# Performance work log

Hardware: AMD Instinct MI355X
Metric: run time of the kernel (lower is better)

## Reference

```python
import jax, jax.numpy as jnp
import numpy as np

H = 256
NUM_REL = 460
NUM_ENT = 20000
B = 4096
CUR_TS = 10
PATH_LEN = 8


def _gru_step(x, h, W_ih, W_hh, b_ih, b_hh):
    # PyTorch GRUCell math
    gi = x @ W_ih.T + b_ih          # [B, 3H]
    gh = h @ W_hh.T + b_hh          # [B, 3H]
    ir, iz, inn = jnp.split(gi, 3, axis=1)
    hr, hz, hn = jnp.split(gh, 3, axis=1)
    r = jax.nn.sigmoid(ir + hr)
    z = jax.nn.sigmoid(iz + hz)
    n = jnp.tanh(inn + r * hn)
    return (1.0 - z) * n + z * h


def setup_inputs() -> dict:
    key = jax.random.key(0)
    ks = jax.random.split(key, 24)
    s = 1.0 / np.sqrt(H)
    f32 = jnp.float32
    d = {
        "pre_emb": jax.random.normal(ks[0], (NUM_ENT, H), f32),
        "r_emb": jax.random.normal(ks[1], (NUM_REL, H), f32),
        "partial_embeding": jax.random.normal(ks[2], (B, CUR_TS * NUM_REL), f32),
        # params (uniform-ish linear init scaled by 1/sqrt(H))
        "W_map1": jax.random.normal(ks[3], (2 * H, H), f32) * s,
        "b_map1": jax.random.normal(ks[4], (2 * H,), f32) * s,
        "W_map2": jax.random.normal(ks[5], (H, 2 * H), f32) * s,
        "b_map2": jax.random.normal(ks[6], (H,), f32) * s,
        "W_h1": jax.random.normal(ks[7], (H, H), f32) * s,
        "b_h1": jax.random.normal(ks[8], (H,), f32) * s,
        "W_h2": jax.random.normal(ks[9], (H, H), f32) * s,
        "b_h2": jax.random.normal(ks[10], (H,), f32) * s,
        "W_attn": jax.random.normal(ks[11], (H, H), f32) * s,
        "b_attn": jax.random.normal(ks[12], (H,), f32) * s,
        "W_align": jax.random.normal(ks[13], (H, H), f32) * s,
        "b_align": jax.random.normal(ks[14], (H,), f32) * s,
        "W_ih": jax.random.normal(ks[15], (3 * H, H), f32) * s,
        "W_hh": jax.random.normal(ks[16], (3 * H, H), f32) * s,
        "b_ih": jax.random.normal(ks[17], (3 * H,), f32) * s,
        "b_hh": jax.random.normal(ks[18], (3 * H,), f32) * s,
        "all_triples": jax.random.randint(ks[19], (B, 3), 0, NUM_REL, dtype=jnp.int64)
        if jax.config.jax_enable_x64 else jax.random.randint(ks[19], (B, 3), 0, NUM_REL, dtype=jnp.int32),
        "cur_ts": CUR_TS,
        "num_rel": NUM_REL,
    }
    return d


def reference(pre_emb, r_emb, partial_embeding,
              W_map1, b_map1, W_map2, b_map2,
              W_h1, b_h1, W_h2, b_h2,
              W_attn, b_attn, W_align, b_align,
              W_ih, W_hh, b_ih, b_hh,
              all_triples, cur_ts, num_rel):
    # rel_mapping1 -> rel_mapping2
    mapped_rel = (r_emb @ W_map1.T + b_map1) @ W_map2.T + b_map2     # [R, H]
    q_rel = mapped_rel[all_triples[:, 1]]                            # [B, H]

    # attention logits base (constant over timesteps): linear_attn(q_rel) @ mapped_rel.T
    attn_base = (q_rel @ W_attn.T + b_attn) @ mapped_rel.T           # [B, R]

    start_ts = max(cur_ts - PATH_LEN, 0)
    nb = partial_embeding.shape[0]
    cur_seq = partial_embeding.reshape(nb, cur_ts, num_rel)[:, start_ts:cur_ts]  # [B, T, R]
    cur_seq = jnp.swapaxes(cur_seq, 0, 1)                            # [T, B, R]

    h0 = jnp.zeros((nb, H), dtype=pre_emb.dtype)

    def step(h, cur):
        attn = cur * attn_base
        attn = jnp.where(attn == 0, jnp.asarray(-1e9, attn.dtype), attn)
        attn = jax.nn.softmax(attn, axis=1)
        x = attn @ mapped_rel                                        # [B, H]
        return _gru_step(x, h, W_ih, W_hh, b_ih, b_hh), None

    gru_hidden, _ = jax.lax.scan(step, h0, cur_seq)

    # predicted history embedding + match loss (MSE)
    predicted_hist = 0.1 * ((q_rel @ W_h1.T + b_h1) @ W_h2.T + b_h2) + q_rel
    match_loss = jnp.mean((predicted_hist - gru_hidden) ** 2)

    # forward_forth, distmult scoring
    h2 = _gru_step(q_rel, predicted_hist, W_ih, W_hh, b_ih, b_hh)    # [B, H]
    aligned_all = pre_emb @ W_align.T + b_align                      # [E, H]
    sub = aligned_all[all_triples[:, 0]]                             # [B, H]
    score_logits = (sub * h2) @ aligned_all.T                        # [B, E]
    score = jax.nn.sigmoid(score_logits)

    # BCE(sigmoid(logits), one_hot(obj)) in stable logits form without
    # materializing the dense one-hot label matrix:
    # mean over B*E of [ softplus(x) - x * label ]
    obj = all_triples[:, 2]
    pos_logits = score_logits[jnp.arange(nb), obj]
    path_loss = (jnp.sum(jax.nn.softplus(score_logits)) - jnp.sum(pos_logits)) / (nb * score_logits.shape[1])

    return match_loss, path_loss, score
```

## Files before the change

### kernel.cpp

```cpp
#include <hip/hip_runtime.h>
#include <hip/hip_bf16.h>

typedef __hip_bfloat16 bf16;
typedef __attribute__((ext_vector_type(8))) short short8;
typedef __attribute__((ext_vector_type(4))) float f32x4;
typedef __attribute__((ext_vector_type(4))) short short4v;

#define NREL 460
#define KP   480
#define NENT 20000
#define NENT_PAD 20096
#define NB   4096

__device__ inline float sigmoidf_(float x){ return 1.f/(1.f+__expf(-x)); }

__device__ inline void gload16(const bf16* g, bf16* l){
  __builtin_amdgcn_global_load_lds(
      (const __attribute__((address_space(1))) unsigned int*)g,
      (__attribute__((address_space(3))) unsigned int*)l, 16, 0, 0);
}

__device__ __forceinline__ void fgemm_body(
    const float* __restrict__ A, int lda, int arows,
    const float* __restrict__ B, int ldb,
    const float* __restrict__ bias,
    float* __restrict__ C, int ldc, int K, int mode,
    const float* __restrict__ add_src, bf16* __restrict__ ct_out,
    int bx, int by)
{
  __shared__ __align__(16) float As[32][68];
  __shared__ __align__(16) float Bs[32][68];
  const int tid = threadIdx.x;
  const int row0 = bx*64, col0 = by*64;
  const int tx = tid & 15, ty = tid >> 4;
  float acc[4][4] = {};
  for (int k0 = 0; k0 < K; k0 += 32){
    __syncthreads();
    #pragma unroll
    for (int s = 0; s < 2; ++s){
      int slot = tid + s*256;
      int r = slot >> 3, c4 = (slot & 7)*4;
      int ra = row0 + r; if (ra >= arows) ra = arows - 1;
      float4 v = *(const float4*)(A + (long)ra*lda + k0 + c4);
      As[c4+0][r] = v.x; As[c4+1][r] = v.y; As[c4+2][r] = v.z; As[c4+3][r] = v.w;
      float4 w = *(const float4*)(B + (long)(col0 + r)*ldb + k0 + c4);
      Bs[c4+0][r] = w.x; Bs[c4+1][r] = w.y; Bs[c4+2][r] = w.z; Bs[c4+3][r] = w.w;
    }
    __syncthreads();
    #pragma unroll
    for (int kk = 0; kk < 32; ++kk){
      float4 a4 = *(const float4*)(&As[kk][ty*4]);
      float4 b4 = *(const float4*)(&Bs[kk][tx*4]);
      float av[4] = {a4.x, a4.y, a4.z, a4.w};
      float bv[4] = {b4.x, b4.y, b4.z, b4.w};
      #pragma unroll
      for (int i = 0; i < 4; ++i)
        #pragma unroll
        for (int j = 0; j < 4; ++j) acc[i][j] += av[i]*bv[j];
    }
  }
  const int rb = row0 + ty*4, cb = col0 + tx*4;
  if (mode == 1){
    #pragma unroll
    for (int i = 0; i < 4; ++i){
      float4 v = {acc[i][0], acc[i][1], acc[i][2], acc[i][3]};
      *(float4*)(C + (long)(rb+i)*ldc + cb) = v;
      int rr = rb + i;
      if (rr < KP){
        #pragma unroll
        for (int j = 0; j < 4; ++j)
          ct_out[(cb+j)*KP + rr] = __float2bfloat16(rr < NREL ? acc[i][j] : 0.f);
      }
    }
  } else if (mode == 2){
    #pragma unroll
    for (int i = 0; i < 4; ++i){
      float4 v;
      #pragma unroll
      for (int j = 0; j < 4; ++j)
        ((float*)&v)[j] = 0.1f*(acc[i][j] + bias[cb+j]) + add_src[(long)(rb+i)*ldc + cb+j];
      *(float4*)(C + (long)(rb+i)*ldc + cb) = v;
    }
  } else {
    float bv[4] = {0,0,0,0};
    if (bias){ bv[0]=bias[cb]; bv[1]=bias[cb+1]; bv[2]=bias[cb+2]; bv[3]=bias[cb+3]; }
    #pragma unroll
    for (int i = 0; i < 4; ++i){
      float4 v = {acc[i][0]+bv[0], acc[i][1]+bv[1], acc[i][2]+bv[2], acc[i][3]+bv[3]};
      *(float4*)(C + (long)(rb+i)*ldc + cb) = v;
    }
  }
}

__global__ __launch_bounds__(256) void k_fgemm(
    const float* A, int lda, int arows, const float* B, int ldb,
    const float* bias, float* C, int ldc, int K, int mode,
    const float* add_src, bf16* ct_out){
  fgemm_body(A, lda, arows, B, ldb, bias, C, ldc, K, mode, add_src, ct_out,
             blockIdx.x, blockIdx.y);
}

struct FDesc {
  const float* A; const float* B; const float* bias; float* C;
  const float* add; bf16* ct;
  int lda, ldb, ldc, K, arows, mode;
};

__global__ __launch_bounds__(256) void k_fgemm_multi(FDesc d0, FDesc d1, FDesc d2,
                                                     int y1, int y2){
  int y = blockIdx.y;
  FDesc d; int by;
  if (y < y1){ d = d0; by = y; }
  else if (y < y2){ d = d1; by = y - y1; }
  else { d = d2; by = y - y2; }
  fgemm_body(d.A, d.lda, d.arows, d.B, d.ldb, d.bias, d.C, d.ldc, d.K, d.mode,
             d.add, d.ct, blockIdx.x, by);
}

__global__ __launch_bounds__(256) void k_h2(const float* __restrict__ M_ih,
    const float* __restrict__ b_ih, const float* __restrict__ ghp,
    const float* __restrict__ ph, float* __restrict__ h2_rel){
  int r = blockIdx.x, c = threadIdx.x;
  float rg = sigmoidf_(M_ih[r*768+c]       + b_ih[c]       + ghp[r*768+c]);
  float zg = sigmoidf_(M_ih[r*768+256+c]   + b_ih[256+c]   + ghp[r*768+256+c]);
  float ng = tanhf    (M_ih[r*768+512+c]   + b_ih[512+c]   + rg*ghp[r*768+512+c]);
  h2_rel[r*256+c] = (1.f - zg)*ng + zg*ph[r*256+c];
}

__global__ void k_f2bf3(const float4* __restrict__ s0, short4v* __restrict__ d0, int n0,
                        const float4* __restrict__ s1, short4v* __restrict__ d1, int n1,
                        const float4* __restrict__ s2, short4v* __restrict__ d2, int n2,
                        short4v* __restrict__ pad0, int n3, double* __restrict__ dz){
  int i = blockIdx.x*256 + threadIdx.x;
  if (i < n0+n1+n2){
    const float4* s; short4v* d; int j;
    if (i < n0){ s = s0; d = d0; j = i; }
    else if (i < n0+n1){ s = s1; d = d1; j = i-n0; }
    else { s = s2; d = d2; j = i-n0-n1; }
    float4 v = s[j];
    bf16 a = __float2bfloat16(v.x), b = __float2bfloat16(v.y);
    bf16 c = __float2bfloat16(v.z), e = __float2bfloat16(v.w);
    short4v o; o.x = *(short*)&a; o.y = *(short*)&b; o.z = *(short*)&c; o.w = *(short*)&e;
    d[j] = o;
  } else if (i < n0+n1+n2+n3){
    short4v z = {0,0,0,0};
    pad0[i - (n0+n1+n2)] = z;
  } else if (i < n0+n1+n2+n3+4){
    dz[i - (n0+n1+n2+n3)] = 0.0;
  }
}

__global__ __launch_bounds__(256) void k_soft_makep(const float* __restrict__ partial,
    const float* __restrict__ attn_base, const int* __restrict__ trips,
    bf16* __restrict__ attn_all,
    const bf16* __restrict__ Qbf, const float* __restrict__ h2_rel,
    bf16* __restrict__ P){
  int bid = blockIdx.x;
  if (bid >= NB/4){
    int i = (bid - NB/4)*256 + threadIdx.x;
    int b = i >> 8, k = i & 255;
    int s = trips[b*3+0], rel = trips[b*3+1];
    P[i] = __float2bfloat16(__bfloat162float(Qbf[s*256+k]) * h2_rel[rel*256+k]);
    return;
  }
  int wave = threadIdx.x >> 6, lane = threadIdx.x & 63;
  int b = bid*4 + wave;
  int rel = trips[b*3+1];
  const float* base = attn_base + (long)rel*512;
  float bs[8];
  #pragma unroll
  for (int s = 0; s < 8; ++s){
    int idx = s*64 + lane;
    bs[s] = (idx < NREL) ? base[idx] : 0.f;
  }
  const float* cur0 = partial + (long)b*4600 + 2*NREL;
  for (int t = 0; t < 8; ++t){
    const float* cur = cur0 + t*NREL;
    float v[8]; float mx = -1e30f;
    #pragma unroll
    for (int s = 0; s < 8; ++s){
      int idx = s*64 + lane;
      float val = -1e30f;
      if (idx < NREL){
        float pz = cur[idx]*bs[s];
        val = (pz == 0.f) ? -1e9f : pz;
      }
      v[s] = val; mx = fmaxf(mx, val);
    }
    #pragma unroll
    for (int off = 32; off >= 1; off >>= 1) mx = fmaxf(mx, __shfl_xor(mx, off));
    float sum = 0.f;
    #pragma unroll
    for (int s = 0; s < 8; ++s){
      int idx = s*64 + lane;
      if (idx < NREL){ v[s] = __expf(v[s]-mx); sum += v[s]; }
    }
    #pragma unroll
    for (int off = 32; off >= 1; off >>= 1) sum += __shfl_xor(sum, off);
    float inv = 1.f/sum;
    long obase = ((long)t*NB + b)*KP;
    #pragma unroll
    for (int s = 0; s < 8; ++s){
      int idx = s*64 + lane;
      if (idx < KP) attn_all[obase + idx] = __float2bfloat16(idx < NREL ? v[s]*inv : 0.f);
    }
  }
}

template<int MODE>
__global__ __launch_bounds__(256) void k_gemm128(
    const bf16* __restrict__ A, int lda,
    const bf16* __restrict__ B, int ldb,
    const float* __restrict__ bias,
    void* __restrict__ C, long ldc,
    int K, int n_valid, double* __restrict__ sp_sum,
    const int* __restrict__ trips)
{
  __shared__ __align__(16) bf16 sbuf[16384];
  __shared__ float wsum[8];
  const int tid = threadIdx.x;
  const int lane = tid & 63, wave = tid >> 6;
  const long row0 = (long)blockIdx.x * 128;
  const long col0 = (long)blockIdx.y * 128;
  const int sr = tid >> 2;
  const int sc = (tid & 3) * 8;
  const bf16* Ag0 = A + (row0 + sr)*lda + sc;
  const bf16* Ag1 = A + (row0 + 64 + sr)*lda + sc;
  const bf16* Bg0 = B + (col0 + sr)*ldb + sc;
  const bf16* Bg1 = B + (col0 + 64 + sr)*ldb + sc;
  const int wr = (wave >> 1)*64, wc = (wave & 1)*64;
  const int rA = lane & 15, kA = (lane >> 4)*8;
  f32x4 acc[4][4] = {};
  const int nt = K >> 5;
  bf16* As_ = sbuf;
  bf16* Bs_ = sbuf + 8192;
  gload16(Ag0, As_ + tid*8);
  gload16(Ag1, As_ + 2048 + tid*8);
  gload16(Bg0, Bs_ + tid*8);
  gload16(Bg1, Bs_ + 2048 + tid*8);
  int cur = 0;
  for (int t = 0; t < nt; ++t){
    if (t + 1 < nt){
      const int k0 = (t+1) << 5;
      const int nxt = cur ^ 1;
      gload16(Ag0 + k0, As_ + nxt*4096 + tid*8);
      gload16(Ag1 + k0, As_ + nxt*4096 + 2048 + tid*8);
      gload16(Bg0 + k0, Bs_ + nxt*4096 + tid*8);
      gload16(Bg1 + k0, Bs_ + nxt*4096 + 2048 + tid*8);
      asm volatile("s_waitcnt vmcnt(4)" ::: "memory");
    } else {
      asm volatile("s_waitcnt vmcnt(0)" ::: "memory");
    }
    __builtin_amdgcn_s_barrier();
    short8 a[4], b[4];
    #pragma unroll
    for (int m = 0; m < 4; ++m) a[m] = *(const short8*)(As_ + cur*4096 + (wr + m*16 + rA)*32 + kA);
    #pragma unroll
    for (int n = 0; n < 4; ++n) b[n] = *(const short8*)(Bs_ + cur*4096 + (wc + n*16 + rA)*32 + kA);
    asm volatile("s_waitcnt lgkmcnt(0)" ::: "memory");
    __builtin_amdgcn_s_barrier();
    #pragma unroll
    for (int m = 0; m < 4; ++m)
      #pragma unroll
      for (int n = 0; n < 4; ++n)
        acc[m][n] = __builtin_amdgcn_mfma_f32_16x16x32_bf16(a[m], b[n], acc[m][n], 0,0,0);
    cur ^= 1;
  }
  const int ri = (lane >> 4)*4, ci = lane & 15;
  __syncthreads();
  if constexpr (MODE == 1){
    bf16* epi = sbuf + wave*1152;
    const int rrow = lane >> 2, q = lane & 3;
    #pragma unroll
    for (int m = 0; m < 4; ++m){
      #pragma unroll
      for (int n = 0; n < 4; ++n){
        long c = col0 + wc + n*16 + ci;
        float bv = bias ? bias[c] : 0.f;
        #pragma unroll
        for (int i = 0; i < 4; ++i)
          epi[(ri+i)*72 + n*16 + ci] = __float2bfloat16(acc[m][n][i] + bv);
      }
      long gr = row0 + wr + m*16 + rrow;
      bf16* gp = (bf16*)C + gr*ldc + col0 + wc + q*16;
      const bf16* lp = epi + rrow*72 + q*16;
      *(short8*)(gp)     = *(const short8*)(lp);
      *(short8*)(gp + 8) = *(const short8*)(lp + 8);
    }
  } else {
    float* epi = (float*)sbuf + wave*1088;
    const int rrow = lane >> 2, q = lane & 3;
    const bool maybe = (col0 + wc) < 464;
    float spart = 0.f, ppart = 0.f;
    #pragma unroll
    for (int m = 0; m < 4; ++m){
      int obj[4];
      if (maybe){
        #pragma unroll
        for (int i = 0; i < 4; ++i)
          obj[i] = trips[3*(int)(row0 + wr + m*16 + ri + i) + 2];
      }
      #pragma unroll
      for (int n = 0; n < 4; ++n){
        long c = col0 + wc + n*16 + ci;
        bool cv = (c < n_valid);
        #pragma unroll
        for (int i = 0; i < 4; ++i){
          float v = acc[m][n][i];
          float sg = 0.f;
          if (cv){
            float e = __expf(-fabsf(v));
            float tt = 1.f + e;
            float rr = __builtin_amdgcn_rcpf(tt);
            sg = (v >= 0.f) ? rr : 1.f - rr;
            spart += fmaxf(v, 0.f) + e*(0.9404f - 0.2537f*e);
            if (maybe && c == obj[i]) ppart += v;
          }
          epi[(ri+i)*68 + n*16 + ci + 2] = sg;
        }
      }
      long gr = row0 + wr + m*16 + rrow;
      long c16 = col0 + wc + q*16;
      if (c16 < n_valid){
        float* gp = (float*)C + gr*ldc + c16;
        const float* lp = epi + rrow*68 + q*16 + 2;
        *(float2*)(gp)      = *(const float2*)(lp);
        *(float4*)(gp + 2)  = *(const float4*)(lp + 2);
        *(float4*)(gp + 6)  = *(const float4*)(lp + 6);
        *(float4*)(gp + 10) = *(const float4*)(lp + 10);
        *(float2*)(gp + 14) = *(const float2*)(lp + 14);
      }
    }
    #pragma unroll
    for (int off = 32; off >= 1; off >>= 1){
      spart += __shfl_xor(spart, off);
      ppart += __shfl_xor(ppart, off);
    }
    if (lane == 0){ wsum[wave] = spart; wsum[4+wave] = ppart; }
    __syncthreads();
    if (tid == 0)
      atomicAdd(sp_sum, (double)(wsum[0]+wsum[1]+wsum[2]+wsum[3]));
    if (tid == 1)
      atomicAdd(sp_sum+1, (double)(wsum[4]+wsum[5]+wsum[6]+wsum[7]));
  }
}

__global__ __launch_bounds__(512) void k_scan(
    const bf16* __restrict__ gi_all,
    const bf16* __restrict__ W_hh_bf,
    const float* __restrict__ b_hh,
    const float* __restrict__ ph,
    const int* __restrict__ trips,
    double* __restrict__ dsum)
{
  __shared__ __align__(16) bf16 hl[16*264];
  __shared__ __align__(16) bf16 gbuf[2][16*768];
  __shared__ float red[8];
  const int tid = threadIdx.x;
  const int lane = tid & 63, wave = tid >> 6;
  const int brow0 = blockIdx.x * 16;
  const int rA = lane & 15, kA = (lane >> 4) * 8;
  const int ci = lane & 15, rbase = (lane >> 4) * 4;
  float hreg[2][4] = {};
  float bh[3][2];
  #pragma unroll
  for (int f = 0; f < 2; ++f){
    int cf = wave*32 + f*16 + ci;
    bh[0][f] = b_hh[cf]; bh[1][f] = b_hh[256+cf]; bh[2][f] = b_hh[512+cf];
  }
  {
    const bf16* src = gi_all + (long)brow0 * 768;
    #pragma unroll
    for (int i = 0; i < 3; ++i){
      int off = (wave*3 + i)*512 + lane*8;
      gload16(src + off, gbuf[0] + off);
    }
  }
  int cur = 0;
  for (int t = 0; t < 8; ++t){
    f32x4 acc[3][2] = {};
    if (t > 0){
      #pragma unroll
      for (int k0 = 0; k0 < 256; k0 += 32){
        short8 a = *(const short8*)(hl + rA*264 + k0 + kA);
        #pragma unroll
        for (int g = 0; g < 3; ++g)
          #pragma unroll
          for (int f = 0; f < 2; ++f){
            int brow = g*256 + wave*32 + f*16 + rA;
            short8 b = *(const short8*)(W_hh_bf + brow*256 + k0 + kA);
            acc[g][f] = __builtin_amdgcn_mfma_f32_16x16x32_bf16(a, b, acc[g][f], 0,0,0);
          }
      }
    }
    asm volatile("s_waitcnt lgkmcnt(0) vmcnt(0)" ::: "memory");
    __builtin_amdgcn_s_barrier();
    if (t < 7){
      const bf16* src = gi_all + ((long)(t+1)*NB + brow0) * 768;
      bf16* dst = gbuf[cur ^ 1];
      #pragma unroll
      for (int i = 0; i < 3; ++i){
        int off = (wave*3 + i)*512 + lane*8;
        gload16(src + off, dst + off);
      }
    }
    const bf16* gl = gbuf[cur];
    #pragma unroll
    for (int f = 0; f < 2; ++f){
      int cf = wave*32 + f*16 + ci;
      #pragma unroll
      for (int i = 0; i < 4; ++i){
        int rloc = rbase + i;
        float gir = __bfloat162float(gl[rloc*768 + cf]);
        float giz = __bfloat162float(gl[rloc*768 + 256 + cf]);
        float gin = __bfloat162float(gl[rloc*768 + 512 + cf]);
        float rg = sigmoidf_(gir + acc[0][f][i] + bh[0][f]);
        float zg = sigmoidf_(giz + acc[1][f][i] + bh[1][f]);
        float ng = tanhf(gin + rg*(acc[2][f][i] + bh[2][f]));
        float hn = (1.f - zg)*ng + zg*hreg[f][i];
        hreg[f][i] = hn;
        hl[rloc*264 + cf] = __float2bfloat16(hn);
      }
    }
    asm volatile("s_waitcnt lgkmcnt(0)" ::: "memory");
    __builtin_amdgcn_s_barrier();
    cur ^= 1;
  }
  float d = 0.f;
  #pragma unroll
  for (int f = 0; f < 2; ++f){
    int cf = wave*32 + f*16 + ci;
    #pragma unroll
    for (int i = 0; i < 4; ++i){
      int rel = trips[(brow0 + rbase + i)*3 + 1];
      float diff = ph[rel*256 + cf] - hreg[f][i];
      d += diff*diff;
    }
  }
  #pragma unroll
  for (int off = 32; off >= 1; off >>= 1) d += __shfl_xor(d, off);
  if (lane == 0) red[wave] = d;
  __syncthreads();
  if (tid == 0){
    float s = 0.f;
    #pragma unroll
    for (int w = 0; w < 8; ++w) s += red[w];
    atomicAdd(dsum, (double)s);
  }
}

__global__ void k_final(const double* __restrict__ d, float* __restrict__ out){
  out[0] = (float)(d[0] / (4096.0*256.0));
  out[1] = (float)((d[1] - d[2]) / (4096.0*20000.0));
}

extern "C" void kernel_launch(void* const* d_in, const int* in_sizes, int n_in,
                              void* d_out, int out_size, void* d_ws, size_t ws_size,
                              hipStream_t stream){
  const float* pre_emb = (const float*)d_in[0];
  const float* r_emb   = (const float*)d_in[1];
  const float* partial = (const float*)d_in[2];
  const float* W_map1  = (const float*)d_in[3];
  const float* b_map1  = (const float*)d_in[4];
  const float* W_map2  = (const float*)d_in[5];
  const float* b_map2  = (const float*)d_in[6];
  const float* W_h1    = (const float*)d_in[7];
  const float* b_h1    = (const float*)d_in[8];
  const float* W_h2    = (const float*)d_in[9];
  const float* b_h2    = (const float*)d_in[10];
  const float* W_attn  = (const float*)d_in[11];
  const float* b_attn  = (const float*)d_in[12];
  const float* W_align = (const float*)d_in[13];
  const float* b_align = (const float*)d_in[14];
  const float* W_ih    = (const float*)d_in[15];
  const float* W_hh    = (const float*)d_in[16];
  const float* b_ih    = (const float*)d_in[17];
  const float* b_hh    = (const float*)d_in[18];
  const int*   trips   = (const int*)d_in[19];
  float* out = (float*)d_out;

  char* w = (char*)d_ws;
  auto alloc = [&](size_t bytes)->char*{
    char* r = w; w += (bytes + 255) & ~size_t(255); return r;
  };
  double* dsum      = (double*)alloc(128);
  float* t1         = (float*)alloc(512*512*4);
  float* mapped     = (float*)alloc(512*256*4);
  float* a1         = (float*)alloc(512*256*4);
  float* th         = (float*)alloc(512*256*4);
  float* ph         = (float*)alloc(512*256*4);
  float* M_ih       = (float*)alloc(512*768*4);
  float* ghp        = (float*)alloc(512*768*4);
  float* attn_base  = (float*)alloc(512*512*4);
  float* h2_rel     = (float*)alloc(NREL*256*4);
  bf16*  M_ihT      = (bf16*)alloc(768*KP*2);
  bf16*  W_hh_bf    = (bf16*)alloc(768*256*2);
  bf16*  W_align_bf = (bf16*)alloc(256*256*2);
  bf16*  Q_bf       = (bf16*)alloc((size_t)NENT_PAD*256*2);
  bf16*  P_bf       = (bf16*)alloc((size_t)NB*256*2);
  bf16*  attn_all   = (bf16*)alloc((size_t)8*NB*KP*2);
  bf16*  gi_all     = (bf16*)alloc((size_t)8*NB*768*2);
  bf16*  pre_bf     = attn_all;

  {
    int n0 = NENT*256/4, n1 = 768*256/4, n2 = 256*256/4;
    int n3 = (NENT_PAD-NENT)*256/4;
    int ntot = n0+n1+n2+n3+4;
    k_f2bf3<<<(ntot+255)/256, 256, 0, stream>>>(
        (const float4*)pre_emb, (short4v*)pre_bf, n0,
        (const float4*)W_hh, (short4v*)W_hh_bf, n1,
        (const float4*)W_align, (short4v*)W_align_bf, n2,
        (short4v*)(pre_bf + (size_t)NENT*256), n3, dsum);
  }

  k_fgemm<<<dim3(8,8),256,0,stream>>>(r_emb,256,NREL, W_map1,256, b_map1, t1,512, 256, 0, nullptr, nullptr);
  k_fgemm<<<dim3(8,4),256,0,stream>>>(t1,512,512, W_map2,512, b_map2, mapped,256, 512, 0, nullptr, nullptr);
  {
    FDesc d0 = { mapped, W_ih,   nullptr, M_ih, nullptr, M_ihT, 256, 256, 768, 256, 512, 1 };
    FDesc d1 = { mapped, W_attn, b_attn,  a1,   nullptr, nullptr, 256, 256, 256, 256, 512, 0 };
    FDesc d2 = { mapped, W_h1,   b_h1,    th,   nullptr, nullptr, 256, 256, 256, 256, 512, 0 };
    k_fgemm_multi<<<dim3(8,20),256,0,stream>>>(d0, d1, d2, 12, 16);
  }
  k_fgemm<<<dim3(8,4),256,0,stream>>>(th,256,512, W_h2,256, b_h2, ph,256, 256, 2, mapped, nullptr);
  {
    FDesc d0 = { a1, mapped, nullptr, attn_base, nullptr, nullptr, 256, 256, 512, 256, 512, 0 };
    FDesc d1 = { ph, W_hh,   b_hh,    ghp,       nullptr, nullptr, 256, 256, 768, 256, 512, 0 };
    k_fgemm_multi<<<dim3(8,20),256,0,stream>>>(d0, d1, d1, 8, 20);
  }
  k_h2<<<NREL,256,0,stream>>>(M_ih, b_ih, ghp, ph, h2_rel);

  {
    dim3 g(NENT_PAD/128, 256/128);
    k_gemm128<1><<<g,256,0,stream>>>(pre_bf, 256, W_align_bf, 256, b_align,
                                     Q_bf, 256, 256, 0, nullptr, nullptr);
  }
  k_soft_makep<<<NB/4 + NB,256,0,stream>>>(partial, attn_base, trips, attn_all,
                                           Q_bf, h2_rel, P_bf);

  {
    dim3 g(8*NB/128, 768/128);
    k_gemm128<1><<<g,256,0,stream>>>(attn_all, KP, M_ihT, KP, b_ih,
                                     gi_all, 768, KP, 0, nullptr, nullptr);
  }

  k_scan<<<NB/16,512,0,stream>>>(gi_all, W_hh_bf, b_hh, ph, trips, dsum);

  {
    dim3 g(NB/128, NENT_PAD/128);
    k_gemm128<2><<<g,256,0,stream>>>(P_bf, 256, Q_bf, 256, nullptr,
                                     out+2, NENT, 256, NENT, dsum+1, trips);
  }
  k_final<<<1,1,0,stream>>>(dsum, out);
}
```

Baseline: 416.9 us.

## Fuse prep kernels into persistent kernel with grid barriers; triple-buffer GEMM

Merges the bf16 conversions, the small fp32 GEMM chain, the h2 gate and the attention softmax into one persistent 256-block kernel that uses atomic-counter grid barriers, replacing about eight separate launches. The P-vector build moves into an extra grid column of the gi GEMM, and the final loss reduction is done by a last-block ticket instead of a separate one-thread kernel. The bf16 GEMM goes from double to triple buffering of its global-to-LDS loads, and the scan kernel keeps most W_hh fragments in registers. The costs are spin-wait barriers that deadlock unless all 256 blocks are co-resident, extra register pressure in the scan, and serialized prep phases that run on few blocks.

Result: slower. 1.000 ms (+140.0%).

```diff
diff --git a/kernel.cpp b/kernel.cpp
--- a/kernel.cpp
+++ b/kernel.cpp
@@ -11,6 +11,7 @@
 #define NENT 20000
 #define NENT_PAD 20096
 #define NB   4096
+#define NBLK 256
 
 __device__ inline float sigmoidf_(float x){ return 1.f/(1.f+__expf(-x)); }
 
@@ -18,6 +19,17 @@
   __builtin_amdgcn_global_load_lds(
       (const __attribute__((address_space(1))) unsigned int*)g,
       (__attribute__((address_space(3))) unsigned int*)l, 16, 0, 0);
+}
+
+__device__ __forceinline__ void gbar(int* cnt){
+  __syncthreads();
+  if (threadIdx.x == 0){
+    __threadfence();
+    atomicAdd(cnt, 1);
+    while (__hip_atomic_load(cnt, __ATOMIC_ACQUIRE, __HIP_MEMORY_SCOPE_AGENT) < NBLK)
+      __builtin_amdgcn_s_sleep(8);
+  }
+  __syncthreads();
 }
 
 __device__ __forceinline__ void fgemm_body(
@@ -92,117 +104,119 @@
   }
 }
 
-__global__ __launch_bounds__(256) void k_fgemm(
-    const float* A, int lda, int arows, const float* B, int ldb,
-    const float* bias, float* C, int ldc, int K, int mode,
-    const float* add_src, bf16* ct_out){
-  fgemm_body(A, lda, arows, B, ldb, bias, C, ldc, K, mode, add_src, ct_out,
-             blockIdx.x, blockIdx.y);
-}
-
-struct FDesc {
-  const float* A; const float* B; const float* bias; float* C;
-  const float* add; bf16* ct;
-  int lda, ldb, ldc, K, arows, mode;
-};
-
-__global__ __launch_bounds__(256) void k_fgemm_multi(FDesc d0, FDesc d1, FDesc d2,
-                                                     int y1, int y2){
-  int y = blockIdx.y;
-  FDesc d; int by;
-  if (y < y1){ d = d0; by = y; }
-  else if (y < y2){ d = d1; by = y - y1; }
-  else { d = d2; by = y - y2; }
-  fgemm_body(d.A, d.lda, d.arows, d.B, d.ldb, d.bias, d.C, d.ldc, d.K, d.mode,
-             d.add, d.ct, blockIdx.x, by);
-}
-
-__global__ __launch_bounds__(256) void k_h2(const float* __restrict__ M_ih,
-    const float* __restrict__ b_ih, const float* __restrict__ ghp,
-    const float* __restrict__ ph, float* __restrict__ h2_rel){
-  int r = blockIdx.x, c = threadIdx.x;
-  float rg = sigmoidf_(M_ih[r*768+c]       + b_ih[c]       + ghp[r*768+c]);
-  float zg = sigmoidf_(M_ih[r*768+256+c]   + b_ih[256+c]   + ghp[r*768+256+c]);
-  float ng = tanhf    (M_ih[r*768+512+c]   + b_ih[512+c]   + rg*ghp[r*768+512+c]);
-  h2_rel[r*256+c] = (1.f - zg)*ng + zg*ph[r*256+c];
-}
-
-__global__ void k_f2bf3(const float4* __restrict__ s0, short4v* __restrict__ d0, int n0,
-                        const float4* __restrict__ s1, short4v* __restrict__ d1, int n1,
-                        const float4* __restrict__ s2, short4v* __restrict__ d2, int n2,
-                        short4v* __restrict__ pad0, int n3, double* __restrict__ dz){
-  int i = blockIdx.x*256 + threadIdx.x;
-  if (i < n0+n1+n2){
-    const float4* s; short4v* d; int j;
-    if (i < n0){ s = s0; d = d0; j = i; }
-    else if (i < n0+n1){ s = s1; d = d1; j = i-n0; }
-    else { s = s2; d = d2; j = i-n0-n1; }
-    float4 v = s[j];
-    bf16 a = __float2bfloat16(v.x), b = __float2bfloat16(v.y);
-    bf16 c = __float2bfloat16(v.z), e = __float2bfloat16(v.w);
-    short4v o; o.x = *(short*)&a; o.y = *(short*)&b; o.z = *(short*)&c; o.w = *(short*)&e;
-    d[j] = o;
-  } else if (i < n0+n1+n2+n3){
-    short4v z = {0,0,0,0};
-    pad0[i - (n0+n1+n2)] = z;
-  } else if (i < n0+n1+n2+n3+4){
-    dz[i - (n0+n1+n2+n3)] = 0.0;
-  }
-}
-
-__global__ __launch_bounds__(256) void k_soft_makep(const float* __restrict__ partial,
-    const float* __restrict__ attn_base, const int* __restrict__ trips,
-    bf16* __restrict__ attn_all,
-    const bf16* __restrict__ Qbf, const float* __restrict__ h2_rel,
-    bf16* __restrict__ P){
-  int bid = blockIdx.x;
-  if (bid >= NB/4){
-    int i = (bid - NB/4)*256 + threadIdx.x;
-    int b = i >> 8, k = i & 255;
-    int s = trips[b*3+0], rel = trips[b*3+1];
-    P[i] = __float2bfloat16(__bfloat162float(Qbf[s*256+k]) * h2_rel[rel*256+k]);
-    return;
-  }
-  int wave = threadIdx.x >> 6, lane = threadIdx.x & 63;
-  int b = bid*4 + wave;
-  int rel = trips[b*3+1];
-  const float* base = attn_base + (long)rel*512;
-  float bs[8];
-  #pragma unroll
-  for (int s = 0; s < 8; ++s){
-    int idx = s*64 + lane;
-    bs[s] = (idx < NREL) ? base[idx] : 0.f;
-  }
-  const float* cur0 = partial + (long)b*4600 + 2*NREL;
-  for (int t = 0; t < 8; ++t){
-    const float* cur = cur0 + t*NREL;
-    float v[8]; float mx = -1e30f;
-    #pragma unroll
-    for (int s = 0; s < 8; ++s){
-      int idx = s*64 + lane;
-      float val = -1e30f;
-      if (idx < NREL){
-        float pz = cur[idx]*bs[s];
-        val = (pz == 0.f) ? -1e9f : pz;
-      }
-      v[s] = val; mx = fmaxf(mx, val);
-    }
-    #pragma unroll
-    for (int off = 32; off >= 1; off >>= 1) mx = fmaxf(mx, __shfl_xor(mx, off));
-    float sum = 0.f;
-    #pragma unroll
-    for (int s = 0; s < 8; ++s){
-      int idx = s*64 + lane;
-      if (idx < NREL){ v[s] = __expf(v[s]-mx); sum += v[s]; }
-    }
-    #pragma unroll
-    for (int off = 32; off >= 1; off >>= 1) sum += __shfl_xor(sum, off);
-    float inv = 1.f/sum;
-    long obase = ((long)t*NB + b)*KP;
-    #pragma unroll
-    for (int s = 0; s < 8; ++s){
-      int idx = s*64 + lane;
-      if (idx < KP) attn_all[obase + idx] = __float2bfloat16(idx < NREL ? v[s]*inv : 0.f);
+__global__ __launch_bounds__(256) void k_prep(
+    const float* __restrict__ r_emb,
+    const float* __restrict__ W_map1, const float* __restrict__ b_map1,
+    const float* __restrict__ W_map2, const float* __restrict__ b_map2,
+    const float* __restrict__ W_ih,
+    const float* __restrict__ W_attn, const float* __restrict__ b_attn,
+    const float* __restrict__ W_h1, const float* __restrict__ b_h1,
+    const float* __restrict__ W_h2, const float* __restrict__ b_h2,
+    const float* __restrict__ W_hh, const float* __restrict__ b_hh,
+    const float* __restrict__ b_ih,
+    const float* __restrict__ pre_emb, const float* __restrict__ W_align,
+    const float* __restrict__ partial, const int* __restrict__ trips,
+    float* t1, float* mapped, float* a1, float* th, float* ph,
+    float* M_ih, float* ghp, float* attn_base, float* h2_rel,
+    bf16* M_ihT, bf16* W_hh_bf, bf16* W_align_bf, bf16* pre_bf,
+    bf16* attn_all, int* cnt)
+{
+  const int tid = threadIdx.x;
+  const int bx = blockIdx.x;
+
+  {
+    const int n0 = NENT*256/4, n1 = 768*256/4, n2 = 256*256/4;
+    const int n3 = (NENT_PAD-NENT)*256/4;
+    for (int i = bx*256 + tid; i < n0+n1+n2+n3; i += NBLK*256){
+      if (i < n0+n1+n2){
+        const float4* s; short4v* d; int j;
+        if (i < n0){ s = (const float4*)pre_emb; d = (short4v*)pre_bf; j = i; }
+        else if (i < n0+n1){ s = (const float4*)W_hh; d = (short4v*)W_hh_bf; j = i-n0; }
+        else { s = (const float4*)W_align; d = (short4v*)W_align_bf; j = i-n0-n1; }
+        float4 v = s[j];
+        bf16 a = __float2bfloat16(v.x), b = __float2bfloat16(v.y);
+        bf16 c = __float2bfloat16(v.z), e = __float2bfloat16(v.w);
+        short4v o; o.x = *(short*)&a; o.y = *(short*)&b; o.z = *(short*)&c; o.w = *(short*)&e;
+        d[j] = o;
+      } else {
+        short4v z = {0,0,0,0};
+        ((short4v*)(pre_bf + (size_t)NENT*256))[i - (n0+n1+n2)] = z;
+      }
+    }
+  }
+  if (bx < 64)
+    fgemm_body(r_emb,256,NREL, W_map1,256, b_map1, t1,512, 256, 0, nullptr,nullptr, bx&7, bx>>3);
+  gbar(cnt+0);
+  if (bx < 32)
+    fgemm_body(t1,512,512, W_map2,512, b_map2, mapped,256, 512, 0, nullptr,nullptr, bx&7, bx>>3);
+  gbar(cnt+1);
+  if (bx < 96)
+    fgemm_body(mapped,256,512, W_ih,256, nullptr, M_ih,768, 256, 1, nullptr, M_ihT, bx&7, bx>>3);
+  else if (bx < 128){ int t = bx-96;
+    fgemm_body(mapped,256,512, W_attn,256, b_attn, a1,256, 256, 0, nullptr,nullptr, t&7, t>>3); }
+  else if (bx < 160){ int t = bx-128;
+    fgemm_body(mapped,256,512, W_h1,256, b_h1, th,256, 256, 0, nullptr,nullptr, t&7, t>>3); }
+  gbar(cnt+2);
+  if (bx < 32)
+    fgemm_body(th,256,512, W_h2,256, b_h2, ph,256, 256, 2, mapped, nullptr, bx&7, bx>>3);
+  else if (bx < 96){ int t = bx-32;
+    fgemm_body(a1,256,512, mapped,256, nullptr, attn_base,512, 256, 0, nullptr,nullptr, t&7, t>>3); }
+  gbar(cnt+3);
+  if (bx < 96)
+    fgemm_body(ph,256,512, W_hh,256, b_hh, ghp,768, 256, 0, nullptr,nullptr, bx&7, bx>>3);
+  gbar(cnt+4);
+  for (int r = bx; r < NREL; r += NBLK){
+    int c = tid;
+    float rg = sigmoidf_(M_ih[r*768+c]     + b_ih[c]     + ghp[r*768+c]);
+    float zg = sigmoidf_(M_ih[r*768+256+c] + b_ih[256+c] + ghp[r*768+256+c]);
+    float ng = tanhf    (M_ih[r*768+512+c] + b_ih[512+c] + rg*ghp[r*768+512+c]);
+    h2_rel[r*256+c] = (1.f - zg)*ng + zg*ph[r*256+c];
+  }
+  gbar(cnt+5);
+  {
+    int wave = tid >> 6, lane = tid & 63;
+    for (int round = 0; round < 4; ++round){
+      int b = round*1024 + bx*4 + wave;
+      int rel = trips[b*3+1];
+      const float* base = attn_base + (long)rel*512;
+      float bs[8];
+      #pragma unroll
+      for (int s = 0; s < 8; ++s){
+        int idx = s*64 + lane;
+        bs[s] = (idx < NREL) ? base[idx] : 0.f;
+      }
+      const float* cur0 = partial + (long)b*4600 + 2*NREL;
+      for (int t = 0; t < 8; ++t){
+        const float* cur = cur0 + t*NREL;
+        float v[8]; float mx = -1e30f;
+        #pragma unroll
+        for (int s = 0; s < 8; ++s){
+          int idx = s*64 + lane;
+          float val = -1e30f;
+          if (idx < NREL){
+            float pz = cur[idx]*bs[s];
+            val = (pz == 0.f) ? -1e9f : pz;
+          }
+          v[s] = val; mx = fmaxf(mx, val);
+        }
+        #pragma unroll
+        for (int off = 32; off >= 1; off >>= 1) mx = fmaxf(mx, __shfl_xor(mx, off));
+        float sum = 0.f;
+        #pragma unroll
+        for (int s = 0; s < 8; ++s){
+          int idx = s*64 + lane;
+          if (idx < NREL){ v[s] = __expf(v[s]-mx); sum += v[s]; }
+        }
+        #pragma unroll
+        for (int off = 32; off >= 1; off >>= 1) sum += __shfl_xor(sum, off);
+        float inv = 1.f/sum;
+        long obase = ((long)t*NB + b)*KP;
+        #pragma unroll
+        for (int s = 0; s < 8; ++s){
+          int idx = s*64 + lane;
+          if (idx < KP) attn_all[obase + idx] = __float2bfloat16(idx < NREL ? v[s]*inv : 0.f);
+        }
+      }
     }
   }
 }
@@ -213,10 +227,27 @@
     const bf16* __restrict__ B, int ldb,
     const float* __restrict__ bias,
     void* __restrict__ C, long ldc,
-    int K, int n_valid, double* __restrict__ sp_sum,
-    const int* __restrict__ trips)
+    int K, int n_valid,
+    double* __restrict__ dsum, const int* __restrict__ trips,
+    const bf16* __restrict__ mp_Q, const float* __restrict__ mp_h2,
+    bf16* __restrict__ mp_P,
+    int* __restrict__ done, float* __restrict__ outf)
 {
-  __shared__ __align__(16) bf16 sbuf[16384];
+  if (MODE == 1 && mp_P != nullptr && blockIdx.y == gridDim.y - 1){
+    int idx16 = blockIdx.x*256 + threadIdx.x;
+    int b = idx16 >> 4, kq = (idx16 & 15) << 4;
+    int s = trips[b*3], rel = trips[b*3+1];
+    const bf16* qr = mp_Q + (long)s*256 + kq;
+    const float* hr = mp_h2 + rel*256 + kq;
+    bf16 outv[16];
+    #pragma unroll
+    for (int j = 0; j < 16; ++j)
+      outv[j] = __float2bfloat16(__bfloat162float(qr[j]) * hr[j]);
+    *(short8*)(mp_P + (long)b*256 + kq)     = *(short8*)(outv);
+    *(short8*)(mp_P + (long)b*256 + kq + 8) = *(short8*)(outv + 8);
+    return;
+  }
+  __shared__ __align__(16) bf16 sbuf[24576];
   __shared__ float wsum[8];
   const int tid = threadIdx.x;
   const int lane = tid & 63, wave = tid >> 6;
@@ -228,25 +259,27 @@
   const bf16* Ag1 = A + (row0 + 64 + sr)*lda + sc;
   const bf16* Bg0 = B + (col0 + sr)*ldb + sc;
   const bf16* Bg1 = B + (col0 + 64 + sr)*ldb + sc;
+  bf16* As_ = sbuf;
+  bf16* Bs_ = sbuf + 12288;
   const int wr = (wave >> 1)*64, wc = (wave & 1)*64;
   const int rA = lane & 15, kA = (lane >> 4)*8;
   f32x4 acc[4][4] = {};
   const int nt = K >> 5;
-  bf16* As_ = sbuf;
-  bf16* Bs_ = sbuf + 8192;
-  gload16(Ag0, As_ + tid*8);
-  gload16(Ag1, As_ + 2048 + tid*8);
-  gload16(Bg0, Bs_ + tid*8);
-  gload16(Bg1, Bs_ + 2048 + tid*8);
+  auto stage = [&](int t, int buf){
+    const int k0 = t << 5;
+    gload16(Ag0 + k0, As_ + buf*4096 + tid*8);
+    gload16(Ag1 + k0, As_ + buf*4096 + 2048 + tid*8);
+    gload16(Bg0 + k0, Bs_ + buf*4096 + tid*8);
+    gload16(Bg1 + k0, Bs_ + buf*4096 + 2048 + tid*8);
+  };
+  stage(0, 0); stage(1, 1);
   int cur = 0;
   for (int t = 0; t < nt; ++t){
-    if (t + 1 < nt){
-      const int k0 = (t+1) << 5;
-      const int nxt = cur ^ 1;
-      gload16(Ag0 + k0, As_ + nxt*4096 + tid*8);
-      gload16(Ag1 + k0, As_ + nxt*4096 + 2048 + tid*8);
-      gload16(Bg0 + k0, Bs_ + nxt*4096 + tid*8);
-      gload16(Bg1 + k0, Bs_ + nxt*4096 + 2048 + tid*8);
+    if (t + 2 < nt){
+      int nb = cur + 2; if (nb >= 3) nb -= 3;
+      stage(t + 2, nb);
+      asm volatile("s_waitcnt vmcnt(8)" ::: "memory");
+    } else if (t + 2 == nt){
       asm volatile("s_waitcnt vmcnt(4)" ::: "memory");
     } else {
       asm volatile("s_waitcnt vmcnt(0)" ::: "memory");
@@ -264,7 +297,7 @@
       #pragma unroll
       for (int n = 0; n < 4; ++n)
         acc[m][n] = __builtin_amdgcn_mfma_f32_16x16x32_bf16(a[m], b[n], acc[m][n], 0,0,0);
-    cur ^= 1;
+    if (++cur == 3) cur = 0;
   }
   const int ri = (lane >> 4)*4, ci = lane & 15;
   __syncthreads();
@@ -338,10 +371,20 @@
     }
     if (lane == 0){ wsum[wave] = spart; wsum[4+wave] = ppart; }
     __syncthreads();
-    if (tid == 0)
-      atomicAdd(sp_sum, (double)(wsum[0]+wsum[1]+wsum[2]+wsum[3]));
-    if (tid == 1)
-      atomicAdd(sp_sum+1, (double)(wsum[4]+wsum[5]+wsum[6]+wsum[7]));
+    if (tid == 0){
+      atomicAdd(&dsum[1], (double)(wsum[0]+wsum[1]+wsum[2]+wsum[3]));
+      atomicAdd(&dsum[2], (double)(wsum[4]+wsum[5]+wsum[6]+wsum[7]));
+      __threadfence();
+      int ticket = atomicAdd(done, 1);
+      if (ticket == (int)(gridDim.x*gridDim.y) - 1){
+        __threadfence();
+        double m  = dsum[0];
+        double sp = dsum[1];
+        double pp = dsum[2];
+        outf[0] = (float)(m / (4096.0*256.0));
+        outf[1] = (float)((sp - pp) / (4096.0*20000.0));
+      }
+    }
   }
 }
 
@@ -368,6 +411,14 @@
     int cf = wave*32 + f*16 + ci;
     bh[0][f] = b_hh[cf]; bh[1][f] = b_hh[256+cf]; bh[2][f] = b_hh[512+cf];
   }
+  short8 warr[3][2][6];
+  #pragma unroll
+  for (int g = 0; g < 3; ++g)
+    #pragma unroll
+    for (int f = 0; f < 2; ++f)
+      #pragma unroll
+      for (int k = 0; k < 6; ++k)
+        warr[g][f][k] = *(const short8*)(W_hh_bf + (g*256 + wave*32 + f*16 + rA)*256 + k*32 + kA);
   {
     const bf16* src = gi_all + (long)brow0 * 768;
     #pragma unroll
@@ -381,14 +432,15 @@
     f32x4 acc[3][2] = {};
     if (t > 0){
       #pragma unroll
-      for (int k0 = 0; k0 < 256; k0 += 32){
-        short8 a = *(const short8*)(hl + rA*264 + k0 + kA);
+      for (int k = 0; k < 8; ++k){
+        short8 a = *(const short8*)(hl + rA*264 + k*32 + kA);
         #pragma unroll
         for (int g = 0; g < 3; ++g)
           #pragma unroll
           for (int f = 0; f < 2; ++f){
-            int brow = g*256 + wave*32 + f*16 + rA;
-            short8 b = *(const short8*)(W_hh_bf + brow*256 + k0 + kA);
+            short8 b;
+            if (k < 6) b = warr[g][f][k];
+            else b = *(const short8*)(W_hh_bf + (g*256 + wave*32 + f*16 + rA)*256 + k*32 + kA);
             acc[g][f] = __builtin_amdgcn_mfma_f32_16x16x32_bf16(a, b, acc[g][f], 0,0,0);
           }
       }
@@ -447,11 +499,6 @@
     for (int w = 0; w < 8; ++w) s += red[w];
     atomicAdd(dsum, (double)s);
   }
-}
-
-__global__ void k_final(const double* __restrict__ d, float* __restrict__ out){
-  out[0] = (float)(d[0] / (4096.0*256.0));
-  out[1] = (float)((d[1] - d[2]) / (4096.0*20000.0));
 }
 
 extern "C" void kernel_launch(void* const* d_in, const int* in_sizes, int n_in,
@@ -483,7 +530,8 @@
   auto alloc = [&](size_t bytes)->char*{
     char* r = w; w += (bytes + 255) & ~size_t(255); return r;
   };
-  double* dsum      = (double*)alloc(128);
+  double* dsum      = (double*)alloc(256);
+  int*    cnt       = (int*)(dsum + 8);
   float* t1         = (float*)alloc(512*512*4);
   float* mapped     = (float*)alloc(512*256*4);
   float* a1         = (float*)alloc(512*256*4);
@@ -496,59 +544,39 @@
   bf16*  M_ihT      = (bf16*)alloc(768*KP*2);
   bf16*  W_hh_bf    = (bf16*)alloc(768*256*2);
   bf16*  W_align_bf = (bf16*)alloc(256*256*2);
+  bf16*  pre_bf     = (bf16*)alloc((size_t)NENT_PAD*256*2);
   bf16*  Q_bf       = (bf16*)alloc((size_t)NENT_PAD*256*2);
   bf16*  P_bf       = (bf16*)alloc((size_t)NB*256*2);
   bf16*  attn_all   = (bf16*)alloc((size_t)8*NB*KP*2);
   bf16*  gi_all     = (bf16*)alloc((size_t)8*NB*768*2);
-  bf16*  pre_bf     = attn_all;
+
+  hipMemsetAsync(dsum, 0, 256, stream);
+
+  k_prep<<<NBLK, 256, 0, stream>>>(
+      r_emb, W_map1, b_map1, W_map2, b_map2, W_ih, W_attn, b_attn,
+      W_h1, b_h1, W_h2, b_h2, W_hh, b_hh, b_ih, pre_emb, W_align,
+      partial, trips,
+      t1, mapped, a1, th, ph, M_ih, ghp, attn_base, h2_rel,
+      M_ihT, W_hh_bf, W_align_bf, pre_bf, attn_all, cnt);
 
   {
-    int n0 = NENT*256/4, n1 = 768*256/4, n2 = 256*256/4;
-    int n3 = (NENT_PAD-NENT)*256/4;
-    int ntot = n0+n1+n2+n3+4;
-    k_f2bf3<<<(ntot+255)/256, 256, 0, stream>>>(
-        (const float4*)pre_emb, (short4v*)pre_bf, n0,
-        (const float4*)W_hh, (short4v*)W_hh_bf, n1,
-        (const float4*)W_align, (short4v*)W_align_bf, n2,
-        (short4v*)(pre_bf + (size_t)NENT*256), n3, dsum);
-  }
-
-  k_fgemm<<<dim3(8,8),256,0,stream>>>(r_emb,256,NREL, W_map1,256, b_map1, t1,512, 256, 0, nullptr, nullptr);
-  k_fgemm<<<dim3(8,4),256,0,stream>>>(t1,512,512, W_map2,512, b_map2, mapped,256, 512, 0, nullptr, nullptr);
+    dim3 g(NENT_PAD/128, 2);
+    k_gemm128<1><<<g,256,0,stream>>>(pre_bf, 256, W_align_bf, 256, b_align,
+                                     Q_bf, 256, 256, 0, nullptr, nullptr,
+                                     nullptr, nullptr, nullptr, nullptr, nullptr);
+  }
   {
-    FDesc d0 = { mapped, W_ih,   nullptr, M_ih, nullptr, M_ihT, 256, 256, 768, 256, 512, 1 };
-    FDesc d1 = { mapped, W_attn, b_attn,  a1,   nullptr, nullptr, 256, 256, 256, 256, 512, 0 };
-    FDesc d2 = { mapped, W_h1,   b_h1,    th,   nullptr, nullptr, 256, 256, 256, 256, 512, 0 };
-    k_fgemm_multi<<<dim3(8,20),256,0,stream>>>(d0, d1, d2, 12, 16);
-  }
-  k_fgemm<<<dim3(8,4),256,0,stream>>>(th,256,512, W_h2,256, b_h2, ph,256, 256, 2, mapped, nullptr);
-  {
-    FDesc d0 = { a1, mapped, nullptr, attn_base, nullptr, nullptr, 256, 256, 512, 256, 512, 0 };
-    FDesc d1 = { ph, W_hh,   b_hh,    ghp,       nullptr, nullptr, 256, 256, 768, 256, 512, 0 };
-    k_fgemm_multi<<<dim3(8,20),256,0,stream>>>(d0, d1, d1, 8, 20);
-  }
-  k_h2<<<NREL,256,0,stream>>>(M_ih, b_ih, ghp, ph, h2_rel);
-
-  {
-    dim3 g(NENT_PAD/128, 256/128);
-    k_gemm128<1><<<g,256,0,stream>>>(pre_bf, 256, W_align_bf, 256, b_align,
-                                     Q_bf, 256, 256, 0, nullptr, nullptr);
-  }
-  k_soft_makep<<<NB/4 + NB,256,0,stream>>>(partial, attn_base, trips, attn_all,
-                                           Q_bf, h2_rel, P_bf);
-
-  {
-    dim3 g(8*NB/128, 768/128);
+    dim3 g(8*NB/128, 7);
     k_gemm128<1><<<g,256,0,stream>>>(attn_all, KP, M_ihT, KP, b_ih,
-                                     gi_all, 768, KP, 0, nullptr, nullptr);
-  }
-
+                                     gi_all, 768, KP, 0, nullptr, trips,
+                                     Q_bf, h2_rel, P_bf, nullptr, nullptr);
+  }
   k_scan<<<NB/16,512,0,stream>>>(gi_all, W_hh_bf, b_hh, ph, trips, dsum);
 
   {
     dim3 g(NB/128, NENT_PAD/128);
     k_gemm128<2><<<g,256,0,stream>>>(P_bf, 256, Q_bf, 256, nullptr,
-                                     out+2, NENT, 256, NENT, dsum+1, trips);
-  }
-  k_final<<<1,1,0,stream>>>(dsum, out);
-}
+                                     out+2, NENT, 256, NENT, dsum, trips,
+                                     nullptr, nullptr, nullptr, cnt+6, out);
+  }
+}
```
